# Kernel tuning notes

Measured on AMD Instinct MI355X. Metric: run time of the kernel, lower is better.

The kernel has to match this reference:

```python
import jax, jax.numpy as jnp
import numpy as np

N, T, DS, DA = 256, 64, 32, 8
D, H, FF = 512, 8, 2048
HD = D // H          # head_dim = 64
IN = DS + DA         # input_dim = 40
EULER_STEPS = 4


def setup_inputs():
    key = jax.random.key(0)
    ks = jax.random.split(key, 12)
    g = lambda k, shape: (jax.random.normal(k, shape) * 0.02).astype(jnp.float32)
    z = lambda *s: jnp.zeros(s, jnp.float32)
    o = lambda *s: jnp.ones(s, jnp.float32)
    return {
        "states": jax.random.normal(ks[0], (N, T, DS), jnp.float32),
        "actions": jax.random.normal(ks[1], (N, T, DA), jnp.float32),
        "time_steps": jnp.cumsum(jax.random.uniform(ks[2], (N, T + 1), jnp.float32, 0.01, 0.1), axis=1),
        "W_ode": g(ks[3], (D, D)), "b_ode": z(D),
        "W_in": g(ks[4], (IN, D)), "b_in": z(D),
        "ln_in_g": o(D), "ln_in_b": z(D),
        "W_q": g(ks[5], (D, D)), "b_q": z(D),
        "W_kv": g(ks[6], (IN + D, 2 * D + H)), "b_kv": z(2 * D + H),
        "W_out": g(ks[7], (D, D)), "b_out": z(D),
        "ln_ff_g": o(D), "ln_ff_b": z(D),
        "W_ff1": g(ks[8], (D, FF)), "b_ff1": z(FF),
        "W_ff2": g(ks[9], (FF, D)), "b_ff2": z(D),
        "W_dec": g(ks[10], (D, DS)), "b_dec": z(DS),
    }


def _ln(x, g, b):
    m = jnp.mean(x, -1, keepdims=True)
    v = jnp.mean((x - m) ** 2, -1, keepdims=True)
    return (x - m) * jax.lax.rsqrt(v + 1e-5) * g + b


def _forward(states, actions, time_steps, W_ode, b_ode, W_in, b_in, ln_in_g, ln_in_b,
             W_q, b_q, W_kv, b_kv, W_out, b_out, ln_ff_g, ln_ff_b,
             W_ff1, b_ff1, W_ff2, b_ff2, W_dec, b_dec):
    n = states.shape[0]
    # teacher forcing path (train=True, eps_decay=0): data_i = cat(states_i, actions_i)
    data_seq = jnp.concatenate([states, actions], -1).transpose(1, 0, 2)  # [T, N, IN]
    dts = (time_steps[:, 1:] - time_steps[:, :-1]).T                      # [T, N]

    def step(carry, xs):
        h1, W2 = carry            # h1: [N, D], W2: [N, H, HD, HD] fast weights
        data, dt = xs
        # integrate latent ODE over per-sample dt (fixed-step Euler, autonomous tanh MLP)
        step_dt = (dt / EULER_STEPS)[:, None]
        for _ in range(EULER_STEPS):
            h1 = h1 + step_dt * jnp.tanh(h1 @ W_ode + b_ode)
        # Hebbian fast-weight update: W2 += lr * v (x) k  (per head)
        x = jnp.concatenate([data, h1], -1)
        kvb = x @ W_kv + b_kv
        k = jax.nn.softmax(kvb[:, :D].reshape(n, H, HD), -1)
        v = jnp.tanh(kvb[:, D:2 * D]).reshape(n, H, HD)
        lr = jax.nn.sigmoid(kvb[:, 2 * D:])                    # [N, H]
        W2 = W2 + lr[:, :, None, None] * jnp.einsum('nhv,nhk->nhvk', v, k)
        # query_fast_weight
        q = _ln(data @ W_in + b_in, ln_in_g, ln_in_b) @ W_q + b_q
        q = jax.nn.softmax(q.reshape(n, H, HD), -1)
        out = jnp.einsum('nhvk,nhk->nhv', W2, q).reshape(n, D)
        out = out @ W_out + b_out
        y = _ln(out, ln_ff_g, ln_ff_b)
        out = jnp.maximum(y @ W_ff1 + b_ff1, 0.0) @ W_ff2 + b_ff2 + out  # FF block + residual
        pred = out @ W_dec + b_dec                              # decoder
        return (out, W2), pred

    h0 = jnp.zeros((n, D), states.dtype)
    W20 = jnp.zeros((n, H, HD, HD), states.dtype)
    _, preds = jax.lax.scan(step, (h0, W20), (data_seq, dts))
    return preds.transpose(1, 0, 2)  # [N, T, DS] predicted next states


def reference(states, actions, time_steps, W_ode, b_ode, W_in, b_in, ln_in_g, ln_in_b,
              W_q, b_q, W_kv, b_kv, W_out, b_out, ln_ff_g, ln_ff_b,
              W_ff1, b_ff1, W_ff2, b_ff2, W_dec, b_dec):
    return _forward(states, actions, time_steps, W_ode, b_ode, W_in, b_in, ln_in_g, ln_in_b,
                    W_q, b_q, W_kv, b_kv, W_out, b_out, ln_ff_g, ln_ff_b,
                    W_ff1, b_ff1, W_ff2, b_ff2, W_dec, b_dec)
```

## Files before the change

### kernel.cpp

```cpp
#include <hip/hip_runtime.h>

#define NS   256
#define TS   64
#define DS   32
#define DA   8
#define DD   512
#define HH   8
#define HD   64
#define FF   2048
#define INP  40
#define INPP 20
#define INPG 24
#define DP   256
#define KVKP 276
#define KVKPP 280
#define KVO  1032
#define FFP  1024

#define OFF_ODE 0
#define SZ_ODE  (32*512*8)
#define OFF_KV  (OFF_ODE+SZ_ODE)
#define SZ_KV   (35*1032*8)
#define OFF_IN  (OFF_KV+SZ_KV)
#define SZ_IN   (3*512*8)
#define OFF_Q   (OFF_IN+SZ_IN)
#define SZ_Q    (32*512*8)
#define OFF_OUT (OFF_Q+SZ_Q)
#define SZ_OUT  (32*512*8)
#define OFF_F1  (OFF_OUT+SZ_OUT)
#define SZ_F1   (32*2048*8)
#define OFF_F2  (OFF_F1+SZ_F1)
#define SZ_F2   (128*512*8)
#define OFF_DEC (OFF_F2+SZ_F2)
#define SZ_DEC  (32*32*8)

#define DEV __device__ __forceinline__

typedef _Float16 half2_t __attribute__((ext_vector_type(2)));

DEV half2_t as_h2(unsigned int u) { return __builtin_bit_cast(half2_t, u); }

DEV float dot2f(unsigned int w, unsigned int x, float acc) {
#if __has_builtin(__builtin_amdgcn_fdot2)
  return __builtin_amdgcn_fdot2(as_h2(w), as_h2(x), acc, false);
#else
  half2_t a = as_h2(w), b = as_h2(x);
  return acc + (float)a[0] * (float)b[0] + (float)a[1] * (float)b[1];
#endif
}

DEV unsigned int pack2f(float a, float b) {
  unsigned short ua = __builtin_bit_cast(unsigned short, (_Float16)a);
  unsigned short ub = __builtin_bit_cast(unsigned short, (_Float16)b);
  return ((unsigned int)ub << 16) | (unsigned int)ua;
}

DEV float fast_tanh(float x) {
  float ax = fabsf(x);
  float e  = __expf(-2.0f * ax);
  float r  = (1.0f - e) / (1.0f + e);
  return copysignf(r, x);
}

DEV float fast_sigmoid(float x) { return 1.0f / (1.0f + __expf(-x)); }

#define LD4(p) (*reinterpret_cast<const uint4*>(p))

DEV float dotG(const unsigned int* __restrict__ Wc, int strideG,
               const unsigned int* __restrict__ xq, int NG, float init) {
  float a0 = init, a1 = 0.f, a2 = 0.f, a3 = 0.f;
  #pragma unroll 4
  for (int g = 0; g < NG; ++g) {
    uint4 w0 = LD4(Wc + g * strideG);
    uint4 w1 = LD4(Wc + g * strideG + 4);
    uint4 x0 = LD4(xq + g * 8);
    uint4 x1 = LD4(xq + g * 8 + 4);
    a0 = dot2f(w0.x, x0.x, a0); a1 = dot2f(w0.y, x0.y, a1);
    a2 = dot2f(w0.z, x0.z, a2); a3 = dot2f(w0.w, x0.w, a3);
    a0 = dot2f(w1.x, x1.x, a0); a1 = dot2f(w1.y, x1.y, a1);
    a2 = dot2f(w1.z, x1.z, a2); a3 = dot2f(w1.w, x1.w, a3);
  }
  return (a0 + a1) + (a2 + a3);
}

__global__ void pack_wg_kernel(const float* __restrict__ src, unsigned int* __restrict__ dst,
                               int K, int KPpad, int Dout) {
  int idx = blockIdx.x * blockDim.x + threadIdx.x;
  int total = KPpad * Dout;
  if (idx >= total) return;
  int kp = idx / Dout;
  int j  = idx - kp * Dout;
  int r0 = 2 * kp, r1 = r0 + 1;
  float lo = (r0 < K) ? src[r0 * Dout + j] : 0.f;
  float hi = (r1 < K) ? src[r1 * Dout + j] : 0.f;
  int kg = kp >> 3, sub = kp & 7;
  dst[((kg * Dout + j) << 3) + sub] = pack2f(lo, hi);
}

__global__ __launch_bounds__(1024, 4) void fwp_main(
    const float* __restrict__ states, const float* __restrict__ actions,
    const float* __restrict__ tsteps,
    const float* __restrict__ b_ode, const float* __restrict__ b_in,
    const float* __restrict__ ln_in_g, const float* __restrict__ ln_in_b,
    const float* __restrict__ b_q, const float* __restrict__ b_kv,
    const float* __restrict__ b_out,
    const float* __restrict__ ln_ff_g, const float* __restrict__ ln_ff_b,
    const float* __restrict__ b_ff1, const float* __restrict__ b_ff2,
    const float* __restrict__ b_dec,
    const unsigned int* __restrict__ Wode, const unsigned int* __restrict__ Wkv,
    const unsigned int* __restrict__ Win,  const unsigned int* __restrict__ Wq,
    const unsigned int* __restrict__ Wout, const unsigned int* __restrict__ Wff1,
    const unsigned int* __restrict__ Wff2, const unsigned int* __restrict__ Wdec,
    unsigned int* __restrict__ ctrs, float* __restrict__ outp) {

  const int n = blockIdx.x, tid = threadIdx.x;
  const int w = tid >> 6, lane = tid & 63;
  const int col = tid & 511;
  const int sub = tid >> 9;
  const int strideG = DD * 8;

  __shared__ alignas(16) float        sh_h[DD];
  __shared__ alignas(16) unsigned int sh_hp[DP];
  __shared__ alignas(16) unsigned int sh_xp[KVKPP];
  __shared__ alignas(16) unsigned int sh_dp[INPG];
  __shared__ alignas(16) float        sh_t[DD];
  __shared__ alignas(16) unsigned int sh_p[DP];
  __shared__ alignas(16) float        sh_kvb[KVO];
  __shared__ alignas(16) float        sh_k[DD];
  __shared__ alignas(16) float        sh_v[DD];
  __shared__ alignas(16) float        sh_q[DD];
  __shared__ float                    sh_lr[HH];
  __shared__ alignas(16) float        sh_ff[FF];
  __shared__ alignas(16) unsigned int sh_ffp[FFP];
  __shared__ float                    sh_red[16];
  __shared__ alignas(16) float        sh_decp[1024];
  __shared__ alignas(16) float        sh_part[512];
  __shared__ int                      sh_flag;

  float W2r[32];
  #pragma unroll
  for (int i = 0; i < 32; ++i) W2r[i] = 0.f;

  if (tid < DD) sh_h[tid] = 0.f;
  if (tid < DP) sh_hp[tid] = 0u;
  if (tid < (KVKPP - KVKP)) sh_xp[KVKP + tid] = 0u;
  if (tid < (INPG - INPP))  sh_dp[INPP + tid] = 0u;

  bool pace = true;
  unsigned int* ctr = ctrs + 16 * (n & 7);

  for (int t = 0; t < TS; ++t) {
    __syncthreads();

    if (pace) {
      if (tid == 0) {
        sh_flag = 0;
        __hip_atomic_fetch_add(ctr, 1u, __ATOMIC_RELAXED, __HIP_MEMORY_SCOPE_AGENT);
        unsigned int tgt = 32u * (unsigned int)(t + 1);
        int it = 0;
        while (__hip_atomic_load(ctr, __ATOMIC_RELAXED, __HIP_MEMORY_SCOPE_AGENT) < tgt) {
          if (++it > 4096) { sh_flag = 1; break; }
          __builtin_amdgcn_s_sleep(8);
        }
      }
      __syncthreads();
      if (sh_flag) pace = false;
    }

    if (tid < INPP) {
      int i0 = 2 * tid, i1 = i0 + 1;
      float a = (i0 < DS) ? states[(n * TS + t) * DS + i0] : actions[(n * TS + t) * DA + (i0 - DS)];
      float c = (i1 < DS) ? states[(n * TS + t) * DS + i1] : actions[(n * TS + t) * DA + (i1 - DS)];
      unsigned int p = pack2f(a, c);
      sh_xp[tid] = p;
      sh_dp[tid] = p;
    }
    const float sdt = 0.25f * (tsteps[n * (TS + 1) + t + 1] - tsteps[n * (TS + 1) + t]);

    for (int e = 0; e < 4; ++e) {
      float acc = dotG(Wode + col * 8 + sub * 16 * strideG, strideG,
                       sh_hp + sub * 128, 16, sub ? 0.f : b_ode[col]);
      if (sub) sh_part[col] = acc;
      __syncthreads();
      if (!sub) sh_h[tid] += sdt * fast_tanh(acc + sh_part[tid]);
      __syncthreads();
      if (tid < DP) sh_hp[tid] = pack2f(sh_h[2 * tid], sh_h[2 * tid + 1]);
      __syncthreads();
    }

    if (tid < DP) sh_xp[INPP + tid] = sh_hp[tid];
    __syncthreads();

    for (int j = tid; j < KVO; j += 1024)
      sh_kvb[j] = dotG(Wkv + j * 8, KVO * 8, sh_xp, 35, b_kv[j]);
    __syncthreads();

    if (tid < DD) {
      float kx = sh_kvb[tid];
      float km = kx;
      #pragma unroll
      for (int o = 32; o; o >>= 1) km = fmaxf(km, __shfl_xor(km, o));
      float ke = __expf(kx - km);
      float ks = ke;
      #pragma unroll
      for (int o = 32; o; o >>= 1) ks += __shfl_xor(ks, o);
      sh_k[tid] = ke / ks;
      sh_v[tid] = fast_tanh(sh_kvb[DD + tid]);
    }
    if (tid < HH) sh_lr[tid] = fast_sigmoid(sh_kvb[2 * DD + tid]);

    {
      float y1 = 0.f;
      if (tid < DD) y1 = dotG(Win + tid * 8, strideG, sh_dp, 3, b_in[tid]);
      float s1 = y1, s2 = y1 * y1;
      #pragma unroll
      for (int o = 32; o; o >>= 1) { s1 += __shfl_xor(s1, o); s2 += __shfl_xor(s2, o); }
      if (tid < DD && lane == 0) { sh_red[2 * w] = s1; sh_red[2 * w + 1] = s2; }
      __syncthreads();
      if (tid < DD) {
        float t1 = 0.f, t2 = 0.f;
        #pragma unroll
        for (int i = 0; i < 8; ++i) { t1 += sh_red[2 * i]; t2 += sh_red[2 * i + 1]; }
        float m  = t1 * (1.0f / DD);
        float va = fmaxf(t2 * (1.0f / DD) - m * m, 0.f);
        float rs = rsqrtf(va + 1e-5f);
        sh_t[tid] = (y1 - m) * rs * ln_in_g[tid] + ln_in_b[tid];
      }
    }
    __syncthreads();
    if (tid < DP) sh_p[tid] = pack2f(sh_t[2 * tid], sh_t[2 * tid + 1]);
    __syncthreads();
    {
      float qacc = dotG(Wq + col * 8 + sub * 16 * strideG, strideG,
                        sh_p + sub * 128, 16, sub ? 0.f : b_q[col]);
      if (sub) sh_part[col] = qacc;
      __syncthreads();
      if (!sub) {
        float qt = qacc + sh_part[tid];
        float qm = qt;
        #pragma unroll
        for (int o = 32; o; o >>= 1) qm = fmaxf(qm, __shfl_xor(qm, o));
        float qe = __expf(qt - qm);
        float qs = qe;
        #pragma unroll
        for (int o = 32; o; o >>= 1) qs += __shfl_xor(qs, o);
        sh_q[tid] = qe / qs;
      }
    }
    __syncthreads();

    {
      int hh = w >> 1, kh = (w & 1) << 5;
      float lv = sh_lr[hh] * sh_v[(hh << 6) + lane];
      float acc = 0.f;
      const float* kb = sh_k + (hh << 6) + kh;
      const float* qb = sh_q + (hh << 6) + kh;
      #pragma unroll
      for (int jc = 0; jc < 8; ++jc) {
        float4 k4 = *reinterpret_cast<const float4*>(kb + 4 * jc);
        float4 q4 = *reinterpret_cast<const float4*>(qb + 4 * jc);
        W2r[4 * jc + 0] += lv * k4.x; acc += W2r[4 * jc + 0] * q4.x;
        W2r[4 * jc + 1] += lv * k4.y; acc += W2r[4 * jc + 1] * q4.y;
        W2r[4 * jc + 2] += lv * k4.z; acc += W2r[4 * jc + 2] * q4.z;
        W2r[4 * jc + 3] += lv * k4.w; acc += W2r[4 * jc + 3] * q4.w;
      }
      if (!(w & 1)) sh_part[(hh << 6) + lane] = acc;
      __syncthreads();
      if (w & 1) sh_t[(hh << 6) + lane] = acc + sh_part[(hh << 6) + lane];
    }
    __syncthreads();
    if (tid < DP) sh_p[tid] = pack2f(sh_t[2 * tid], sh_t[2 * tid + 1]);
    __syncthreads();

    float o1 = 0.f;
    {
      float oacc = dotG(Wout + col * 8 + sub * 16 * strideG, strideG,
                        sh_p + sub * 128, 16, sub ? 0.f : b_out[col]);
      if (sub) sh_part[col] = oacc;
      __syncthreads();
      if (!sub) o1 = oacc + sh_part[tid];
    }

    {
      float s1 = o1, s2 = o1 * o1;
      #pragma unroll
      for (int o = 32; o; o >>= 1) { s1 += __shfl_xor(s1, o); s2 += __shfl_xor(s2, o); }
      if (tid < DD && lane == 0) { sh_red[2 * w] = s1; sh_red[2 * w + 1] = s2; }
      __syncthreads();
      if (tid < DD) {
        float t1 = 0.f, t2 = 0.f;
        #pragma unroll
        for (int i = 0; i < 8; ++i) { t1 += sh_red[2 * i]; t2 += sh_red[2 * i + 1]; }
        float m  = t1 * (1.0f / DD);
        float va = fmaxf(t2 * (1.0f / DD) - m * m, 0.f);
        float rs = rsqrtf(va + 1e-5f);
        sh_t[tid] = (o1 - m) * rs * ln_ff_g[tid] + ln_ff_b[tid];
      }
    }
    __syncthreads();
    if (tid < DP) sh_p[tid] = pack2f(sh_t[2 * tid], sh_t[2 * tid + 1]);
    __syncthreads();

    {
      float f0 = b_ff1[tid], f1 = b_ff1[tid + 1024];
      #pragma unroll 2
      for (int g = 0; g < 32; ++g) {
        const unsigned int* wb = Wff1 + g * (FF * 8) + tid * 8;
        uint4 w00 = LD4(wb);
        uint4 w01 = LD4(wb + 4);
        uint4 w10 = LD4(wb + 1024 * 8);
        uint4 w11 = LD4(wb + 1024 * 8 + 4);
        uint4 x0 = LD4(sh_p + g * 8);
        uint4 x1 = LD4(sh_p + g * 8 + 4);
        f0 = dot2f(w00.x, x0.x, f0); f0 = dot2f(w00.y, x0.y, f0);
        f0 = dot2f(w00.z, x0.z, f0); f0 = dot2f(w00.w, x0.w, f0);
        f0 = dot2f(w01.x, x1.x, f0); f0 = dot2f(w01.y, x1.y, f0);
        f0 = dot2f(w01.z, x1.z, f0); f0 = dot2f(w01.w, x1.w, f0);
        f1 = dot2f(w10.x, x0.x, f1); f1 = dot2f(w10.y, x0.y, f1);
        f1 = dot2f(w10.z, x0.z, f1); f1 = dot2f(w10.w, x0.w, f1);
        f1 = dot2f(w11.x, x1.x, f1); f1 = dot2f(w11.y, x1.y, f1);
        f1 = dot2f(w11.z, x1.z, f1); f1 = dot2f(w11.w, x1.w, f1);
      }
      sh_ff[tid]        = fmaxf(f0, 0.f);
      sh_ff[tid + 1024] = fmaxf(f1, 0.f);
    }
    __syncthreads();
    sh_ffp[tid] = pack2f(sh_ff[2 * tid], sh_ff[2 * tid + 1]);
    __syncthreads();

    {
      float oacc = dotG(Wff2 + col * 8 + sub * 64 * strideG, strideG,
                        sh_ffp + sub * 512, 64, sub ? 0.f : b_ff2[col]);
      if (sub) sh_part[col] = oacc;
      __syncthreads();
      if (!sub) sh_h[tid] = oacc + sh_part[tid] + o1;
    }
    __syncthreads();
    if (tid < DP) sh_hp[tid] = pack2f(sh_h[2 * tid], sh_h[2 * tid + 1]);
    __syncthreads();

    {
      int colD = tid & 31, ch = tid >> 5;
      const unsigned int* wb = Wdec + colD * 8 + ch * (DS * 8);
      uint4 w0 = LD4(wb);
      uint4 w1 = LD4(wb + 4);
      uint4 x0 = LD4(sh_hp + ch * 8);
      uint4 x1 = LD4(sh_hp + ch * 8 + 4);
      float a = 0.f;
      a = dot2f(w0.x, x0.x, a); a = dot2f(w0.y, x0.y, a);
      a = dot2f(w0.z, x0.z, a); a = dot2f(w0.w, x0.w, a);
      a = dot2f(w1.x, x1.x, a); a = dot2f(w1.y, x1.y, a);
      a = dot2f(w1.z, x1.z, a); a = dot2f(w1.w, x1.w, a);
      sh_decp[tid] = a;
    }
    __syncthreads();
    if (tid < DS) {
      float s = b_dec[tid];
      #pragma unroll
      for (int c = 0; c < 32; ++c) s += sh_decp[c * 32 + tid];
      outp[(n * TS + t) * DS + tid] = s;
    }
  }
}

extern "C" void kernel_launch(void* const* d_in, const int* in_sizes, int n_in,
                              void* d_out, int out_size, void* d_ws, size_t ws_size,
                              hipStream_t stream) {
  (void)in_sizes; (void)n_in; (void)out_size; (void)ws_size;

  const float* states   = (const float*)d_in[0];
  const float* actions  = (const float*)d_in[1];
  const float* tsteps   = (const float*)d_in[2];
  const float* W_ode    = (const float*)d_in[3];
  const float* b_ode    = (const float*)d_in[4];
  const float* W_in     = (const float*)d_in[5];
  const float* b_in     = (const float*)d_in[6];
  const float* ln_in_g  = (const float*)d_in[7];
  const float* ln_in_b  = (const float*)d_in[8];
  const float* W_q      = (const float*)d_in[9];
  const float* b_q      = (const float*)d_in[10];
  const float* W_kv     = (const float*)d_in[11];
  const float* b_kv     = (const float*)d_in[12];
  const float* W_out    = (const float*)d_in[13];
  const float* b_out    = (const float*)d_in[14];
  const float* ln_ff_g  = (const float*)d_in[15];
  const float* ln_ff_b  = (const float*)d_in[16];
  const float* W_ff1    = (const float*)d_in[17];
  const float* b_ff1    = (const float*)d_in[18];
  const float* W_ff2    = (const float*)d_in[19];
  const float* b_ff2    = (const float*)d_in[20];
  const float* W_dec    = (const float*)d_in[21];
  const float* b_dec    = (const float*)d_in[22];

  unsigned int* wsbase = (unsigned int*)d_ws;
  unsigned int* ctrs   = wsbase;
  unsigned int* W      = wsbase + 128;

  hipMemsetAsync(d_ws, 0, 512, stream);

  auto launch_pack = [&](const float* src, unsigned int* dst, int K, int KPpad, int Dout) {
    int total = KPpad * Dout;
    int blocks = (total + 255) / 256;
    pack_wg_kernel<<<blocks, 256, 0, stream>>>(src, dst, K, KPpad, Dout);
  };

  launch_pack(W_ode, W + OFF_ODE, 512,  256, 512);
  launch_pack(W_kv,  W + OFF_KV,  552,  280, 1032);
  launch_pack(W_in,  W + OFF_IN,  40,   24,  512);
  launch_pack(W_q,   W + OFF_Q,   512,  256, 512);
  launch_pack(W_out, W + OFF_OUT, 512,  256, 512);
  launch_pack(W_ff1, W + OFF_F1,  512,  256, 2048);
  launch_pack(W_ff2, W + OFF_F2,  2048, 1024, 512);
  launch_pack(W_dec, W + OFF_DEC, 512,  256, 32);

  fwp_main<<<NS, 1024, 0, stream>>>(
      states, actions, tsteps,
      b_ode, b_in, ln_in_g, ln_in_b, b_q, b_kv, b_out, ln_ff_g, ln_ff_b,
      b_ff1, b_ff2, b_dec,
      W + OFF_ODE, W + OFF_KV, W + OFF_IN, W + OFF_Q,
      W + OFF_OUT, W + OFF_F1, W + OFF_F2, W + OFF_DEC,
      ctrs, (float*)d_out);
}
```

Baseline: 6.665 ms.

## Process two samples per block so each weight load feeds both samples

Each 1024-thread block now handles two batch samples instead of one, halving the grid to 128 blocks. Half-wave pairs (lanes 0-31 and 32-63) share the same weight column but use different sample activations, so each global weight fetch serves two samples and the split-K partial-sum exchanges disappear. In exchange, the per-thread fast-weight register array doubles to 64 floats, each thread runs full-length dot products, and only 128 blocks occupy the device. The cross-block pacing target is halved to match.

```diff
diff --git a/kernel.cpp b/kernel.cpp
--- a/kernel.cpp
+++ b/kernel.cpp
@@ -1,6 +1,7 @@
 #include <hip/hip_runtime.h>
 
 #define NS   256
+#define NB   128
 #define TS   64
 #define DS   32
 #define DA   8
@@ -8,7 +9,6 @@
 #define HH   8
 #define HD   64
 #define FF   2048
-#define INP  40
 #define INPP 20
 #define INPG 24
 #define DP   256
@@ -66,7 +66,7 @@
 
 #define LD4(p) (*reinterpret_cast<const uint4*>(p))
 
-DEV float dotG(const unsigned int* __restrict__ Wc, int strideG,
+DEV float dotM(const unsigned int* __restrict__ Wc, int strideG,
                const unsigned int* __restrict__ xq, int NG, float init) {
   float a0 = init, a1 = 0.f, a2 = 0.f, a3 = 0.f;
   #pragma unroll 4
@@ -113,41 +113,43 @@
     const unsigned int* __restrict__ Wff2, const unsigned int* __restrict__ Wdec,
     unsigned int* __restrict__ ctrs, float* __restrict__ outp) {
 
-  const int n = blockIdx.x, tid = threadIdx.x;
+  const int b = blockIdx.x, tid = threadIdx.x;
   const int w = tid >> 6, lane = tid & 63;
-  const int col = tid & 511;
-  const int sub = tid >> 9;
+  const int s1 = lane >> 5;
+  const int mcol = w * 32 + (lane & 31);
+  const int s2 = tid >> 9;
+  const int c2 = tid & 511;
+  const int n0 = 2 * b;
   const int strideG = DD * 8;
 
-  __shared__ alignas(16) float        sh_h[DD];
-  __shared__ alignas(16) unsigned int sh_hp[DP];
-  __shared__ alignas(16) unsigned int sh_xp[KVKPP];
-  __shared__ alignas(16) unsigned int sh_dp[INPG];
-  __shared__ alignas(16) float        sh_t[DD];
-  __shared__ alignas(16) unsigned int sh_p[DP];
-  __shared__ alignas(16) float        sh_kvb[KVO];
-  __shared__ alignas(16) float        sh_k[DD];
-  __shared__ alignas(16) float        sh_v[DD];
-  __shared__ alignas(16) float        sh_q[DD];
-  __shared__ float                    sh_lr[HH];
-  __shared__ alignas(16) float        sh_ff[FF];
-  __shared__ alignas(16) unsigned int sh_ffp[FFP];
-  __shared__ float                    sh_red[16];
-  __shared__ alignas(16) float        sh_decp[1024];
-  __shared__ alignas(16) float        sh_part[512];
+  __shared__ alignas(16) float        sh_h[2][DD];
+  __shared__ alignas(16) unsigned int sh_hp[2][DP];
+  __shared__ alignas(16) unsigned int sh_xp[2][KVKPP];
+  __shared__ alignas(16) unsigned int sh_dp[2][INPG];
+  __shared__ alignas(16) float        sh_t[2][DD];
+  __shared__ alignas(16) unsigned int sh_p[2][DP];
+  __shared__ alignas(16) float        sh_kvb[2][KVO];
+  __shared__ alignas(16) float        sh_k[2][DD];
+  __shared__ alignas(16) float        sh_v[2][DD];
+  __shared__ alignas(16) float        sh_q[2][DD];
+  __shared__ float                    sh_lr[2][HH];
+  __shared__ alignas(16) float        sh_ff[2][FF];
+  __shared__ alignas(16) unsigned int sh_ffp[2][FFP];
+  __shared__ float                    sh_red[2][32];
+  __shared__ alignas(16) float        sh_decp[2][512];
   __shared__ int                      sh_flag;
 
-  float W2r[32];
+  float W2r[64];
   #pragma unroll
-  for (int i = 0; i < 32; ++i) W2r[i] = 0.f;
-
-  if (tid < DD) sh_h[tid] = 0.f;
-  if (tid < DP) sh_hp[tid] = 0u;
-  if (tid < (KVKPP - KVKP)) sh_xp[KVKP + tid] = 0u;
-  if (tid < (INPG - INPP))  sh_dp[INPP + tid] = 0u;
+  for (int i = 0; i < 64; ++i) W2r[i] = 0.f;
+
+  sh_h[s2][c2] = 0.f;
+  if (c2 < DP) sh_hp[s2][c2] = 0u;
+  if (c2 < (KVKPP - KVKP)) sh_xp[s2][KVKP + c2] = 0u;
+  if (c2 < (INPG - INPP))  sh_dp[s2][INPP + c2] = 0u;
 
   bool pace = true;
-  unsigned int* ctr = ctrs + 16 * (n & 7);
+  unsigned int* ctr = ctrs + 16 * (b & 7);
 
   for (int t = 0; t < TS; ++t) {
     __syncthreads();
@@ -156,7 +158,7 @@
       if (tid == 0) {
         sh_flag = 0;
         __hip_atomic_fetch_add(ctr, 1u, __ATOMIC_RELAXED, __HIP_MEMORY_SCOPE_AGENT);
-        unsigned int tgt = 32u * (unsigned int)(t + 1);
+        unsigned int tgt = 16u * (unsigned int)(t + 1);
         int it = 0;
         while (__hip_atomic_load(ctr, __ATOMIC_RELAXED, __HIP_MEMORY_SCOPE_AGENT) < tgt) {
           if (++it > 4096) { sh_flag = 1; break; }
@@ -167,36 +169,40 @@
       if (sh_flag) pace = false;
     }
 
-    if (tid < INPP) {
-      int i0 = 2 * tid, i1 = i0 + 1;
+    if (c2 < INPP) {
+      int n = n0 + s2;
+      int i0 = 2 * c2, i1 = i0 + 1;
       float a = (i0 < DS) ? states[(n * TS + t) * DS + i0] : actions[(n * TS + t) * DA + (i0 - DS)];
       float c = (i1 < DS) ? states[(n * TS + t) * DS + i1] : actions[(n * TS + t) * DA + (i1 - DS)];
       unsigned int p = pack2f(a, c);
-      sh_xp[tid] = p;
-      sh_dp[tid] = p;
-    }
-    const float sdt = 0.25f * (tsteps[n * (TS + 1) + t + 1] - tsteps[n * (TS + 1) + t]);
+      sh_xp[s2][c2] = p;
+      sh_dp[s2][c2] = p;
+    }
+    const float sdtA = 0.25f * (tsteps[n0 * (TS + 1) + t + 1] - tsteps[n0 * (TS + 1) + t]);
+    const float sdtB = 0.25f * (tsteps[(n0 + 1) * (TS + 1) + t + 1] - tsteps[(n0 + 1) * (TS + 1) + t]);
+    const float sdt_s = s1 ? sdtB : sdtA;
 
     for (int e = 0; e < 4; ++e) {
-      float acc = dotG(Wode + col * 8 + sub * 16 * strideG, strideG,
-                       sh_hp + sub * 128, 16, sub ? 0.f : b_ode[col]);
-      if (sub) sh_part[col] = acc;
+      float acc = dotM(Wode + mcol * 8, strideG, sh_hp[s1], 32, b_ode[mcol]);
+      sh_h[s1][mcol] += sdt_s * fast_tanh(acc);
       __syncthreads();
-      if (!sub) sh_h[tid] += sdt * fast_tanh(acc + sh_part[tid]);
+      if (c2 < DP) sh_hp[s2][c2] = pack2f(sh_h[s2][2 * c2], sh_h[s2][2 * c2 + 1]);
       __syncthreads();
-      if (tid < DP) sh_hp[tid] = pack2f(sh_h[2 * tid], sh_h[2 * tid + 1]);
-      __syncthreads();
-    }
-
-    if (tid < DP) sh_xp[INPP + tid] = sh_hp[tid];
-    __syncthreads();
-
-    for (int j = tid; j < KVO; j += 1024)
-      sh_kvb[j] = dotG(Wkv + j * 8, KVO * 8, sh_xp, 35, b_kv[j]);
-    __syncthreads();
-
-    if (tid < DD) {
-      float kx = sh_kvb[tid];
+    }
+
+    if (c2 < DP) sh_xp[s2][INPP + c2] = sh_hp[s2][c2];
+    __syncthreads();
+
+    {
+      sh_kvb[s1][mcol]       = dotM(Wkv + mcol * 8,         KVO * 8, sh_xp[s1], 35, b_kv[mcol]);
+      sh_kvb[s1][mcol + 512] = dotM(Wkv + (mcol + 512) * 8, KVO * 8, sh_xp[s1], 35, b_kv[mcol + 512]);
+      if (mcol < 8)
+        sh_kvb[s1][mcol + 1024] = dotM(Wkv + (mcol + 1024) * 8, KVO * 8, sh_xp[s1], 35, b_kv[mcol + 1024]);
+    }
+    __syncthreads();
+
+    {
+      float kx = sh_kvb[s2][c2];
       float km = kx;
       #pragma unroll
       for (int o = 32; o; o >>= 1) km = fmaxf(km, __shfl_xor(km, o));
@@ -204,59 +210,53 @@
       float ks = ke;
       #pragma unroll
       for (int o = 32; o; o >>= 1) ks += __shfl_xor(ks, o);
-      sh_k[tid] = ke / ks;
-      sh_v[tid] = fast_tanh(sh_kvb[DD + tid]);
-    }
-    if (tid < HH) sh_lr[tid] = fast_sigmoid(sh_kvb[2 * DD + tid]);
-
-    {
-      float y1 = 0.f;
-      if (tid < DD) y1 = dotG(Win + tid * 8, strideG, sh_dp, 3, b_in[tid]);
-      float s1 = y1, s2 = y1 * y1;
-      #pragma unroll
-      for (int o = 32; o; o >>= 1) { s1 += __shfl_xor(s1, o); s2 += __shfl_xor(s2, o); }
-      if (tid < DD && lane == 0) { sh_red[2 * w] = s1; sh_red[2 * w + 1] = s2; }
+      sh_k[s2][c2] = ke / ks;
+      sh_v[s2][c2] = fast_tanh(sh_kvb[s2][DD + c2]);
+      if (c2 < HH) sh_lr[s2][c2] = fast_sigmoid(sh_kvb[s2][2 * DD + c2]);
+    }
+
+    {
+      float y1 = dotM(Win + mcol * 8, strideG, sh_dp[s1], 3, b_in[mcol]);
+      float ss = y1, sq = y1 * y1;
+      #pragma unroll
+      for (int o = 16; o; o >>= 1) { ss += __shfl_xor(ss, o); sq += __shfl_xor(sq, o); }
+      if ((lane & 31) == 0) { sh_red[s1][2 * w] = ss; sh_red[s1][2 * w + 1] = sq; }
       __syncthreads();
-      if (tid < DD) {
-        float t1 = 0.f, t2 = 0.f;
-        #pragma unroll
-        for (int i = 0; i < 8; ++i) { t1 += sh_red[2 * i]; t2 += sh_red[2 * i + 1]; }
-        float m  = t1 * (1.0f / DD);
-        float va = fmaxf(t2 * (1.0f / DD) - m * m, 0.f);
-        float rs = rsqrtf(va + 1e-5f);
-        sh_t[tid] = (y1 - m) * rs * ln_in_g[tid] + ln_in_b[tid];
-      }
-    }
-    __syncthreads();
-    if (tid < DP) sh_p[tid] = pack2f(sh_t[2 * tid], sh_t[2 * tid + 1]);
-    __syncthreads();
-    {
-      float qacc = dotG(Wq + col * 8 + sub * 16 * strideG, strideG,
-                        sh_p + sub * 128, 16, sub ? 0.f : b_q[col]);
-      if (sub) sh_part[col] = qacc;
-      __syncthreads();
-      if (!sub) {
-        float qt = qacc + sh_part[tid];
-        float qm = qt;
-        #pragma unroll
-        for (int o = 32; o; o >>= 1) qm = fmaxf(qm, __shfl_xor(qm, o));
-        float qe = __expf(qt - qm);
-        float qs = qe;
-        #pragma unroll
-        for (int o = 32; o; o >>= 1) qs += __shfl_xor(qs, o);
-        sh_q[tid] = qe / qs;
-      }
-    }
-    __syncthreads();
-
-    {
-      int hh = w >> 1, kh = (w & 1) << 5;
-      float lv = sh_lr[hh] * sh_v[(hh << 6) + lane];
+      float t1 = 0.f, t2 = 0.f;
+      #pragma unroll
+      for (int i = 0; i < 16; ++i) { t1 += sh_red[s1][2 * i]; t2 += sh_red[s1][2 * i + 1]; }
+      float m  = t1 * (1.0f / DD);
+      float va = fmaxf(t2 * (1.0f / DD) - m * m, 0.f);
+      float rs = rsqrtf(va + 1e-5f);
+      sh_t[s1][mcol] = (y1 - m) * rs * ln_in_g[mcol] + ln_in_b[mcol];
+    }
+    __syncthreads();
+    if (c2 < DP) sh_p[s2][c2] = pack2f(sh_t[s2][2 * c2], sh_t[s2][2 * c2 + 1]);
+    __syncthreads();
+
+    sh_t[s1][mcol] = dotM(Wq + mcol * 8, strideG, sh_p[s1], 32, b_q[mcol]);
+    __syncthreads();
+    {
+      float qt = sh_t[s2][c2];
+      float qm = qt;
+      #pragma unroll
+      for (int o = 32; o; o >>= 1) qm = fmaxf(qm, __shfl_xor(qm, o));
+      float qe = __expf(qt - qm);
+      float qs = qe;
+      #pragma unroll
+      for (int o = 32; o; o >>= 1) qs += __shfl_xor(qs, o);
+      sh_q[s2][c2] = qe / qs;
+    }
+    __syncthreads();
+
+    {
+      int head = c2 >> 6;
+      float lv = sh_lr[s2][head] * sh_v[s2][c2];
       float acc = 0.f;
-      const float* kb = sh_k + (hh << 6) + kh;
-      const float* qb = sh_q + (hh << 6) + kh;
-      #pragma unroll
-      for (int jc = 0; jc < 8; ++jc) {
+      const float* kb = sh_k[s2] + head * HD;
+      const float* qb = sh_q[s2] + head * HD;
+      #pragma unroll
+      for (int jc = 0; jc < 16; ++jc) {
         float4 k4 = *reinterpret_cast<const float4*>(kb + 4 * jc);
         float4 q4 = *reinterpret_cast<const float4*>(qb + 4 * jc);
         W2r[4 * jc + 0] += lv * k4.x; acc += W2r[4 * jc + 0] * q4.x;
@@ -264,101 +264,107 @@
         W2r[4 * jc + 2] += lv * k4.z; acc += W2r[4 * jc + 2] * q4.z;
         W2r[4 * jc + 3] += lv * k4.w; acc += W2r[4 * jc + 3] * q4.w;
       }
-      if (!(w & 1)) sh_part[(hh << 6) + lane] = acc;
+      sh_t[s2][c2] = acc;
+    }
+    __syncthreads();
+    if (c2 < DP) sh_p[s2][c2] = pack2f(sh_t[s2][2 * c2], sh_t[s2][2 * c2 + 1]);
+    __syncthreads();
+
+    float o1 = dotM(Wout + mcol * 8, strideG, sh_p[s1], 32, b_out[mcol]);
+    {
+      float ss = o1, sq = o1 * o1;
+      #pragma unroll
+      for (int o = 16; o; o >>= 1) { ss += __shfl_xor(ss, o); sq += __shfl_xor(sq, o); }
+      if ((lane & 31) == 0) { sh_red[s1][2 * w] = ss; sh_red[s1][2 * w + 1] = sq; }
       __syncthreads();
-      if (w & 1) sh_t[(hh << 6) + lane] = acc + sh_part[(hh << 6) + lane];
-    }
-    __syncthreads();
-    if (tid < DP) sh_p[tid] = pack2f(sh_t[2 * tid], sh_t[2 * tid + 1]);
-    __syncthreads();
-
-    float o1 = 0.f;
-    {
-      float oacc = dotG(Wout + col * 8 + sub * 16 * strideG, strideG,
-                        sh_p + sub * 128, 16, sub ? 0.f : b_out[col]);
-      if (sub) sh_part[col] = oacc;
-      __syncthreads();
-      if (!sub) o1 = oacc + sh_part[tid];
-    }
-
-    {
-      float s1 = o1, s2 = o1 * o1;
-      #pragma unroll
-      for (int o = 32; o; o >>= 1) { s1 += __shfl_xor(s1, o); s2 += __shfl_xor(s2, o); }
-      if (tid < DD && lane == 0) { sh_red[2 * w] = s1; sh_red[2 * w + 1] = s2; }
-      __syncthreads();
-      if (tid < DD) {
-        float t1 = 0.f, t2 = 0.f;
-        #pragma unroll
-        for (int i = 0; i < 8; ++i) { t1 += sh_red[2 * i]; t2 += sh_red[2 * i + 1]; }
-        float m  = t1 * (1.0f / DD);
-        float va = fmaxf(t2 * (1.0f / DD) - m * m, 0.f);
-        float rs = rsqrtf(va + 1e-5f);
-        sh_t[tid] = (o1 - m) * rs * ln_ff_g[tid] + ln_ff_b[tid];
-      }
-    }
-    __syncthreads();
-    if (tid < DP) sh_p[tid] = pack2f(sh_t[2 * tid], sh_t[2 * tid + 1]);
-    __syncthreads();
-
-    {
-      float f0 = b_ff1[tid], f1 = b_ff1[tid + 1024];
+      float t1 = 0.f, t2 = 0.f;
+      #pragma unroll
+      for (int i = 0; i < 16; ++i) { t1 += sh_red[s1][2 * i]; t2 += sh_red[s1][2 * i + 1]; }
+      float m  = t1 * (1.0f / DD);
+      float va = fmaxf(t2 * (1.0f / DD) - m * m, 0.f);
+      float rs = rsqrtf(va + 1e-5f);
+      sh_t[s1][mcol] = (o1 - m) * rs * ln_ff_g[mcol] + ln_ff_b[mcol];
+    }
+    __syncthreads();
+    if (c2 < DP) sh_p[s2][c2] = pack2f(sh_t[s2][2 * c2], sh_t[s2][2 * c2 + 1]);
+    __syncthreads();
+
+    {
+      float f0 = b_ff1[mcol];
+      float f1 = b_ff1[mcol + 512];
+      float f2 = b_ff1[mcol + 1024];
+      float f3 = b_ff1[mcol + 1536];
       #pragma unroll 2
       for (int g = 0; g < 32; ++g) {
-        const unsigned int* wb = Wff1 + g * (FF * 8) + tid * 8;
-        uint4 w00 = LD4(wb);
-        uint4 w01 = LD4(wb + 4);
-        uint4 w10 = LD4(wb + 1024 * 8);
-        uint4 w11 = LD4(wb + 1024 * 8 + 4);
-        uint4 x0 = LD4(sh_p + g * 8);
-        uint4 x1 = LD4(sh_p + g * 8 + 4);
-        f0 = dot2f(w00.x, x0.x, f0); f0 = dot2f(w00.y, x0.y, f0);
-        f0 = dot2f(w00.z, x0.z, f0); f0 = dot2f(w00.w, x0.w, f0);
-        f0 = dot2f(w01.x, x1.x, f0); f0 = dot2f(w01.y, x1.y, f0);
-        f0 = dot2f(w01.z, x1.z, f0); f0 = dot2f(w01.w, x1.w, f0);
-        f1 = dot2f(w10.x, x0.x, f1); f1 = dot2f(w10.y, x0.y, f1);
-        f1 = dot2f(w10.z, x0.z, f1); f1 = dot2f(w10.w, x0.w, f1);
-        f1 = dot2f(w11.x, x1.x, f1); f1 = dot2f(w11.y, x1.y, f1);
-        f1 = dot2f(w11.z, x1.z, f1); f1 = dot2f(w11.w, x1.w, f1);
+        const unsigned int* wb = Wff1 + g * (FF * 8) + mcol * 8;
+        uint4 wa0 = LD4(wb);
+        uint4 wa1 = LD4(wb + 4);
+        uint4 wb0 = LD4(wb + 512 * 8);
+        uint4 wb1 = LD4(wb + 512 * 8 + 4);
+        uint4 wc0 = LD4(wb + 1024 * 8);
+        uint4 wc1 = LD4(wb + 1024 * 8 + 4);
+        uint4 wd0 = LD4(wb + 1536 * 8);
+        uint4 wd1 = LD4(wb + 1536 * 8 + 4);
+        uint4 x0 = LD4(sh_p[s1] + g * 8);
+        uint4 x1 = LD4(sh_p[s1] + g * 8 + 4);
+        f0 = dot2f(wa0.x, x0.x, f0); f0 = dot2f(wa0.y, x0.y, f0);
+        f0 = dot2f(wa0.z, x0.z, f0); f0 = dot2f(wa0.w, x0.w, f0);
+        f0 = dot2f(wa1.x, x1.x, f0); f0 = dot2f(wa1.y, x1.y, f0);
+        f0 = dot2f(wa1.z, x1.z, f0); f0 = dot2f(wa1.w, x1.w, f0);
+        f1 = dot2f(wb0.x, x0.x, f1); f1 = dot2f(wb0.y, x0.y, f1);
+        f1 = dot2f(wb0.z, x0.z, f1); f1 = dot2f(wb0.w, x0.w, f1);
+        f1 = dot2f(wb1.x, x1.x, f1); f1 = dot2f(wb1.y, x1.y, f1);
+        f1 = dot2f(wb1.z, x1.z, f1); f1 = dot2f(wb1.w, x1.w, f1);
+        f2 = dot2f(wc0.x, x0.x, f2); f2 = dot2f(wc0.y, x0.y, f2);
+        f2 = dot2f(wc0.z, x0.z, f2); f2 = dot2f(wc0.w, x0.w, f2);
+        f2 = dot2f(wc1.x, x1.x, f2); f2 = dot2f(wc1.y, x1.y, f2);
+        f2 = dot2f(wc1.z, x1.z, f2); f2 = dot2f(wc1.w, x1.w, f2);
+        f3 = dot2f(wd0.x, x0.x, f3); f3 = dot2f(wd0.y, x0.y, f3);
+        f3 = dot2f(wd0.z, x0.z, f3); f3 = dot2f(wd0.w, x0.w, f3);
+        f3 = dot2f(wd1.x, x1.x, f3); f3 = dot2f(wd1.y, x1.y, f3);
+        f3 = dot2f(wd1.z, x1.z, f3); f3 = dot2f(wd1.w, x1.w, f3);
       }
-      sh_ff[tid]        = fmaxf(f0, 0.f);
-      sh_ff[tid + 1024] = fmaxf(f1, 0.f);
-    }
-    __syncthreads();
-    sh_ffp[tid] = pack2f(sh_ff[2 * tid], sh_ff[2 * tid + 1]);
-    __syncthreads();
-
-    {
-      float oacc = dotG(Wff2 + col * 8 + sub * 64 * strideG, strideG,
-                        sh_ffp + sub * 512, 64, sub ? 0.f : b_ff2[col]);
-      if (sub) sh_part[col] = oacc;
-      __syncthreads();
-      if (!sub) sh_h[tid] = oacc + sh_part[tid] + o1;
-    }
-    __syncthreads();
-    if (tid < DP) sh_hp[tid] = pack2f(sh_h[2 * tid], sh_h[2 * tid + 1]);
-    __syncthreads();
-
-    {
-      int colD = tid & 31, ch = tid >> 5;
-      const unsigned int* wb = Wdec + colD * 8 + ch * (DS * 8);
-      uint4 w0 = LD4(wb);
-      uint4 w1 = LD4(wb + 4);
-      uint4 x0 = LD4(sh_hp + ch * 8);
-      uint4 x1 = LD4(sh_hp + ch * 8 + 4);
+      sh_ff[s1][mcol]        = fmaxf(f0, 0.f);
+      sh_ff[s1][mcol + 512]  = fmaxf(f1, 0.f);
+      sh_ff[s1][mcol + 1024] = fmaxf(f2, 0.f);
+      sh_ff[s1][mcol + 1536] = fmaxf(f3, 0.f);
+    }
+    __syncthreads();
+    sh_ffp[s2][c2]       = pack2f(sh_ff[s2][2 * c2], sh_ff[s2][2 * c2 + 1]);
+    sh_ffp[s2][c2 + 512] = pack2f(sh_ff[s2][1024 + 2 * c2], sh_ff[s2][1025 + 2 * c2]);
+    __syncthreads();
+
+    {
+      float o2 = dotM(Wff2 + mcol * 8, strideG, sh_ffp[s1], 128, b_ff2[mcol]);
+      sh_h[s1][mcol] = o2 + o1;
+    }
+    __syncthreads();
+    if (c2 < DP) sh_hp[s2][c2] = pack2f(sh_h[s2][2 * c2], sh_h[s2][2 * c2 + 1]);
+    __syncthreads();
+
+    {
+      int colD = c2 & 31, ch = c2 >> 5;
+      const unsigned int* wbse = Wdec + colD * 8;
       float a = 0.f;
-      a = dot2f(w0.x, x0.x, a); a = dot2f(w0.y, x0.y, a);
-      a = dot2f(w0.z, x0.z, a); a = dot2f(w0.w, x0.w, a);
-      a = dot2f(w1.x, x1.x, a); a = dot2f(w1.y, x1.y, a);
-      a = dot2f(w1.z, x1.z, a); a = dot2f(w1.w, x1.w, a);
-      sh_decp[tid] = a;
-    }
-    __syncthreads();
-    if (tid < DS) {
-      float s = b_dec[tid];
-      #pragma unroll
-      for (int c = 0; c < 32; ++c) s += sh_decp[c * 32 + tid];
-      outp[(n * TS + t) * DS + tid] = s;
+      #pragma unroll
+      for (int g = 2 * ch; g < 2 * ch + 2; ++g) {
+        uint4 w0 = LD4(wbse + g * (DS * 8));
+        uint4 w1 = LD4(wbse + g * (DS * 8) + 4);
+        uint4 x0 = LD4(sh_hp[s2] + g * 8);
+        uint4 x1 = LD4(sh_hp[s2] + g * 8 + 4);
+        a = dot2f(w0.x, x0.x, a); a = dot2f(w0.y, x0.y, a);
+        a = dot2f(w0.z, x0.z, a); a = dot2f(w0.w, x0.w, a);
+        a = dot2f(w1.x, x1.x, a); a = dot2f(w1.y, x1.y, a);
+        a = dot2f(w1.z, x1.z, a); a = dot2f(w1.w, x1.w, a);
+      }
+      sh_decp[s2][c2] = a;
+    }
+    __syncthreads();
+    if (c2 < DS) {
+      float s = b_dec[c2];
+      #pragma unroll
+      for (int c = 0; c < 16; ++c) s += sh_decp[s2][c * 32 + c2];
+      outp[((n0 + s2) * TS + t) * DS + c2] = s;
     }
   }
 }
@@ -413,7 +419,7 @@
   launch_pack(W_ff2, W + OFF_F2,  2048, 1024, 512);
   launch_pack(W_dec, W + OFF_DEC, 512,  256, 32);
 
-  fwp_main<<<NS, 1024, 0, stream>>>(
+  fwp_main<<<NB, 1024, 0, stream>>>(
       states, actions, tsteps,
       b_ode, b_in, ln_in_g, ln_in_b, b_q, b_kv, b_out, ln_ff_g, ln_ff_b,
       b_ff1, b_ff2, b_dec,
```

New measurement: 11.44 ms. 71.7% more time.
